# Kernel tuning notes

Hardware: AMD Instinct MI355X
Metric: run time of the kernel (lower is better)

## Reference

```python
import jax, jax.numpy as jnp
import numpy as np
from jax import lax

B, H, W = 10, 320, 1024
PTS, DENSE, WD, KMEAN = 500, 2000, 11, 10
N = B * PTS  # 5000 center rows


def setup_inputs() -> dict:
    key = jax.random.key(0)
    k1, k2, k3, k4, k5, k6 = jax.random.split(key, 6)
    disp = jax.random.uniform(k1, (B, 1, H, W), dtype=jnp.float32)
    # forepred is a binary foreground prediction map -> strong Sobel edges
    forepred = jnp.round(jax.random.uniform(k2, (B, 1, H, W), dtype=jnp.float32))
    centerx = jax.random.randint(k3, (N,), WD, W - WD, dtype=jnp.int32)
    centery = jax.random.randint(k4, (N,), WD, H - WD, dtype=jnp.int32)
    bx = jax.random.randint(k5, (N, DENSE), -WD, WD + 1, dtype=jnp.int32)
    by = jax.random.randint(k6, (N, DENSE), -7, 8, dtype=jnp.int32)
    return {"disp": disp, "forepred": forepred, "centerx": centerx,
            "centery": centery, "bx": bx, "by": by}


def _mask_grad(disp, forepred):
    # Sobel-x conv, padding=1, no bias
    wx = jnp.array([[-1., 0., 1.], [-2., 0., 2.], [-1., 0., 1.]],
                   dtype=forepred.dtype)[None, None]  # [1,1,3,3]
    g = lax.conv_general_dilated(forepred, wx, (1, 1), 'SAME')
    mg = jnp.abs(g)
    # 3x3 max-pool, stride 1, padding 1 ("expand")
    mg = lax.reduce_window(mg, -jnp.inf, lax.max, (1, 1, 3, 3), (1, 1, 1, 1), 'SAME')
    mg = mg * (disp > 0.007).astype(mg.dtype)
    mg = jnp.maximum(mg, 3.0) - 3.0  # clamp(min=3) - 3
    # zero 4-pixel borders (zeroArea = [0,1,2,3,-1,-2,-3,-4])
    zy = jnp.array([0, 1, 2, 3, H - 1, H - 2, H - 3, H - 4])
    zx = jnp.array([0, 1, 2, 3, W - 1, W - 2, W - 3, W - 4])
    mg = mg.at[:, :, zy, :].set(0.0)
    mg = mg.at[:, :, :, zx].set(0.0)
    return mg


def reference(disp, forepred, centerx, centery, bx, by):
    maskGrad = _mask_grad(disp, forepred)
    channelInd = jnp.repeat(jnp.arange(B, dtype=jnp.int32), PTS)  # [N]
    # on-border row validity (original compacts; we mask instead, jit-friendly)
    validRow = maskGrad[channelInd, 0, centery, centerx] > 0.1  # [N]

    sampledx = centerx[:, None] + bx  # [N, DENSE]
    sampledy = centery[:, None] + by
    flat = (channelInd[:, None].astype(jnp.int32) * H + sampledy) * W + sampledx
    sampledDisp = disp.reshape(-1)[flat]  # irregular gather, [N, DENSE]

    kmeanLarge = jnp.max(sampledDisp, axis=1, keepdims=True)
    kmeanSmall = jnp.min(sampledDisp, axis=1, keepdims=True)
    for _ in range(KMEAN):
        distLarge = jnp.abs(sampledDisp - kmeanLarge)
        distSmall = jnp.abs(sampledDisp - kmeanSmall)
        belongingLarge = (distLarge <= distSmall).astype(sampledDisp.dtype)
        belongingSmall = 1.0 - belongingLarge
        kmeanLarge = (jnp.sum(sampledDisp * belongingLarge, axis=1, keepdims=True)
                      / jnp.sum(belongingLarge, axis=1, keepdims=True))
        kmeanSmall = (jnp.sum(sampledDisp * belongingSmall, axis=1, keepdims=True)
                      / jnp.sum(belongingSmall, axis=1, keepdims=True))

    contrast = ((kmeanLarge - kmeanSmall)[:, 0] > 0.005) & \
               (jnp.sum(belongingLarge, axis=1) > 5)
    keep = (validRow & contrast).astype(sampledDisp.dtype)  # [N]
    # per-row [large, small] cluster means; rows failing selection zeroed
    out = jnp.concatenate([kmeanLarge, kmeanSmall], axis=1) * keep[:, None]
    return out
```

## Files before the change

kernel.cpp:

```cpp
#include <hip/hip_runtime.h>

namespace {

constexpr int Bn    = 10;
constexpr int H     = 320;
constexpr int W     = 1024;
constexpr int PTS   = 500;
constexpr int DENSE = 2000;
constexpr int N     = Bn * PTS;
constexpr int HWp   = H * W;
constexpr int KITER = 10;
constexpr int RPB   = 4;

constexpr int WY   = 15;
constexpr int WX   = 24;
constexpr int WSZ  = WY * WX;
constexpr int WOFF = 7 * WX + 11;

__global__ __launch_bounds__(256, 4)
void rsbsp_kernel(const float* __restrict__ disp,
                  const float* __restrict__ forepred,
                  const int*   __restrict__ centerx,
                  const int*   __restrict__ centery,
                  const int*   __restrict__ bx,
                  const int*   __restrict__ by,
                  float*       __restrict__ out)
{
    __shared__ float win[RPB][WSZ];

    const int wid  = threadIdx.x >> 6;
    const int lane = threadIdx.x & 63;
    const int row  = blockIdx.x * RPB + wid;
    const int b    = row / PTS;
    const int cx   = centerx[row];
    const int cy   = centery[row];
    const float* db = disp     + b * HWp;
    const float* fb = forepred + b * HWp;

    float v = 0.f;
    if (lane < 9) {
        const int dy = lane / 3, dx = lane % 3;
        const float* fp = fb + (cy - 2 + dy) * W + (cx - 2 + dx);
        const float g = (fp[2]         - fp[0])
                + 2.f * (fp[W + 2]     - fp[W])
                +       (fp[2 * W + 2] - fp[2 * W]);
        v = fabsf(g);
    }
    #pragma unroll
    for (int m = 1; m < 16; m <<= 1) v = fmaxf(v, __shfl_xor(v, m));
    v = __shfl(v, 0, 64);

    const float dcen = db[cy * W + cx];
    const float mgv  = fmaxf(v * ((dcen > 0.007f) ? 1.f : 0.f), 3.f) - 3.f;
    const bool validRow = mgv > 0.1f;

    if (!validRow) {
        if (lane == 0) { out[row * 2 + 0] = 0.f; out[row * 2 + 1] = 0.f; }
        return;
    }

    float* wl = win[wid];
    const int gbase = (cy - 7) * W + (cx - 11);
    #pragma unroll
    for (int i = 0; i < 6; ++i) {
        const int w = lane + 64 * i;
        if (w < WSZ) {
            const unsigned r = (unsigned)w / 24u;
            const unsigned c = (unsigned)w - r * 24u;
            wl[w] = db[gbase + r * W + c];
        }
    }

    const int4* bx4 = reinterpret_cast<const int4*>(bx + row * DENSE);
    const int4* by4 = reinterpret_cast<const int4*>(by + row * DENSE);

    float s[32];
    float mx = -INFINITY, mn = INFINITY, tot = 0.f;
    #pragma unroll
    for (int k = 0; k < 8; ++k) {
        const int q = lane + 64 * k;
        if (q < DENSE / 4) {
            const int4 xb = bx4[q];
            const int4 yb = by4[q];
            const float x0 = wl[yb.x * WX + xb.x + WOFF];
            const float x1 = wl[yb.y * WX + xb.y + WOFF];
            const float x2 = wl[yb.z * WX + xb.z + WOFF];
            const float x3 = wl[yb.w * WX + xb.w + WOFF];
            s[k * 4 + 0] = x0; s[k * 4 + 1] = x1;
            s[k * 4 + 2] = x2; s[k * 4 + 3] = x3;
            mx = fmaxf(fmaxf(fmaxf(mx, x0), fmaxf(x1, x2)), x3);
            mn = fminf(fminf(fminf(mn, x0), fminf(x1, x2)), x3);
            tot += (x0 + x1) + (x2 + x3);
        } else {
            s[k * 4 + 0] = -INFINITY; s[k * 4 + 1] = -INFINITY;
            s[k * 4 + 2] = -INFINITY; s[k * 4 + 3] = -INFINITY;
        }
    }

    #pragma unroll
    for (int m = 1; m < 64; m <<= 1) {
        mx  = fmaxf(mx, __shfl_xor(mx, m));
        mn  = fminf(mn, __shfl_xor(mn, m));
        tot += __shfl_xor(tot, m);
    }

    float mL = mx, mS = mn;
    float cntLast = 0.f;
    float prevSum = -1.f, prevCnt = -1.f;
    #pragma unroll 1
    for (int it = 0; it < KITER; ++it) {
        const float mid = 0.5f * (mL + mS);
        float sumL = 0.f;
        int   cw   = 0;
        #pragma unroll
        for (int j = 0; j < 32; ++j) {
            const float x  = s[j];
            const bool  bl = x >= mid;
            sumL += bl ? x : 0.f;
            cw   += (int)__popcll(__ballot(bl));
        }
        #pragma unroll
        for (int m = 1; m < 64; m <<= 1) sumL += __shfl_xor(sumL, m);

        const float cf = (float)cw;
        const float df = (float)DENSE - cf;
        const bool done = (it == KITER - 1) || (cf == prevCnt && sumL == prevSum);
        if (done) {
            mL = sumL / cf;
            mS = (tot - sumL) / df;
            if (cw == DENSE) mS = __int_as_float(0x7fc00000);
            cntLast = cf;
            break;
        }
        mL = sumL * __builtin_amdgcn_rcpf(cf);
        mS = (tot - sumL) * __builtin_amdgcn_rcpf(df);
        prevSum = sumL; prevCnt = cf;
    }

    if (lane == 0) {
        const bool contrast = ((mL - mS) > 0.005f) && (cntLast > 5.f);
        const float keep = contrast ? 1.f : 0.f;
        out[row * 2 + 0] = mL * keep;
        out[row * 2 + 1] = mS * keep;
    }
}

}

extern "C" void kernel_launch(void* const* d_in, const int* in_sizes, int n_in,
                              void* d_out, int out_size, void* d_ws, size_t ws_size,
                              hipStream_t stream) {
    const float* disp = (const float*)d_in[0];
    const float* fore = (const float*)d_in[1];
    const int*   cx   = (const int*)d_in[2];
    const int*   cy   = (const int*)d_in[3];
    const int*   bxp  = (const int*)d_in[4];
    const int*   byp  = (const int*)d_in[5];
    float* out = (float*)d_out;

    rsbsp_kernel<<<N / RPB, 256, 0, stream>>>(disp, fore, cx, cy, bxp, byp, out);
}
```

Measured before the change: 125.6 us.

## Split validity check into separate kernel that writes flags for kmeans kernel

```diff
diff --git a/kernel.cpp b/kernel.cpp
--- a/kernel.cpp
+++ b/kernel.cpp
@@ -17,47 +17,70 @@
 constexpr int WSZ  = WY * WX;
 constexpr int WOFF = 7 * WX + 11;
 
+__global__ __launch_bounds__(256)
+void validity_kernel(const float* __restrict__ disp,
+                     const float* __restrict__ forepred,
+                     const int*   __restrict__ centerx,
+                     const int*   __restrict__ centery,
+                     int*         __restrict__ flags,
+                     float*       __restrict__ out)
+{
+    const int row = blockIdx.x * 256 + threadIdx.x;
+    if (row >= N) return;
+    const int b  = row / PTS;
+    const int cx = centerx[row];
+    const int cy = centery[row];
+    const float* fb = forepred + b * HWp;
+
+    float F[5][5];
+    #pragma unroll
+    for (int a = 0; a < 5; ++a)
+        #pragma unroll
+        for (int c = 0; c < 5; ++c)
+            F[a][c] = fb[(cy - 2 + a) * W + (cx - 2 + c)];
+
+    float v = 0.f;
+    #pragma unroll
+    for (int dy = 0; dy < 3; ++dy)
+        #pragma unroll
+        for (int dx = 0; dx < 3; ++dx) {
+            const float g = (F[dy    ][dx + 2] - F[dy    ][dx])
+                    + 2.f * (F[dy + 1][dx + 2] - F[dy + 1][dx])
+                    +       (F[dy + 2][dx + 2] - F[dy + 2][dx]);
+            v = fmaxf(v, fabsf(g));
+        }
+    const float dcen = disp[b * HWp + cy * W + cx];
+    const float mgv  = fmaxf(v * ((dcen > 0.007f) ? 1.f : 0.f), 3.f) - 3.f;
+    const bool valid = mgv > 0.1f;
+
+    flags[row] = valid ? 1 : 0;
+    if (!valid) {
+        out[row * 2 + 0] = 0.f;
+        out[row * 2 + 1] = 0.f;
+    }
+}
+
 __global__ __launch_bounds__(256, 4)
-void rsbsp_kernel(const float* __restrict__ disp,
-                  const float* __restrict__ forepred,
-                  const int*   __restrict__ centerx,
-                  const int*   __restrict__ centery,
-                  const int*   __restrict__ bx,
-                  const int*   __restrict__ by,
-                  float*       __restrict__ out)
+void kmeans_kernel(const float* __restrict__ disp,
+                   const int*   __restrict__ centerx,
+                   const int*   __restrict__ centery,
+                   const int*   __restrict__ bx,
+                   const int*   __restrict__ by,
+                   const int*   __restrict__ flags,
+                   float*       __restrict__ out)
 {
     __shared__ float win[RPB][WSZ];
 
     const int wid  = threadIdx.x >> 6;
     const int lane = threadIdx.x & 63;
     const int row  = blockIdx.x * RPB + wid;
-    const int b    = row / PTS;
-    const int cx   = centerx[row];
-    const int cy   = centery[row];
-    const float* db = disp     + b * HWp;
-    const float* fb = forepred + b * HWp;
 
-    float v = 0.f;
-    if (lane < 9) {
-        const int dy = lane / 3, dx = lane % 3;
-        const float* fp = fb + (cy - 2 + dy) * W + (cx - 2 + dx);
-        const float g = (fp[2]         - fp[0])
-                + 2.f * (fp[W + 2]     - fp[W])
-                +       (fp[2 * W + 2] - fp[2 * W]);
-        v = fabsf(g);
-    }
-    #pragma unroll
-    for (int m = 1; m < 16; m <<= 1) v = fmaxf(v, __shfl_xor(v, m));
-    v = __shfl(v, 0, 64);
+    if (flags[row] == 0) return;
 
-    const float dcen = db[cy * W + cx];
-    const float mgv  = fmaxf(v * ((dcen > 0.007f) ? 1.f : 0.f), 3.f) - 3.f;
-    const bool validRow = mgv > 0.1f;
-
-    if (!validRow) {
-        if (lane == 0) { out[row * 2 + 0] = 0.f; out[row * 2 + 1] = 0.f; }
-        return;
-    }
+    const int b  = row / PTS;
+    const int cx = centerx[row];
+    const int cy = centery[row];
+    const float* db = disp + b * HWp;
 
     float* wl = win[wid];
     const int gbase = (cy - 7) * W + (cx - 11);
@@ -156,7 +179,9 @@
     const int*   cy   = (const int*)d_in[3];
     const int*   bxp  = (const int*)d_in[4];
     const int*   byp  = (const int*)d_in[5];
-    float* out = (float*)d_out;
+    float* out  = (float*)d_out;
+    int* flags  = (int*)d_ws;
 
-    rsbsp_kernel<<<N / RPB, 256, 0, stream>>>(disp, fore, cx, cy, bxp, byp, out);
+    validity_kernel<<<(N + 255) / 256, 256, 0, stream>>>(disp, fore, cx, cy, flags, out);
+    kmeans_kernel<<<N / RPB, 256, 0, stream>>>(disp, cx, cy, bxp, byp, flags, out);
 }
```

Result: slower. 133.8 us (+6.5%).
